# Kernel optimization log

Hardware: AMD Instinct MI355X
Metric: run time of the kernel (lower is better)

Reference implementation:

```python
import jax, jax.numpy as jnp
import numpy as np

HIDDEN = 2048
NUM_HEADS = 16
HEAD_DIM = HIDDEN // NUM_HEADS
ROPE_THETA = 10000.0


def _rope_cos_sin(n, dtype):
    # Llama-style: inv_freq over even indices, emb = concat([freqs, freqs])
    inv_freq = 1.0 / (ROPE_THETA ** (jnp.arange(0, HEAD_DIM, 2, dtype=jnp.float32) / HEAD_DIM))
    pos = jnp.arange(n, dtype=jnp.float32)
    freqs = pos[:, None] * inv_freq[None, :]          # [N, HEAD_DIM/2]
    emb = jnp.concatenate([freqs, freqs], axis=-1)    # [N, HEAD_DIM]
    return jnp.cos(emb).astype(dtype), jnp.sin(emb).astype(dtype)


def _rotate_half(x):
    x1, x2 = jnp.split(x, 2, axis=-1)
    return jnp.concatenate([-x2, x1], axis=-1)


def setup_inputs() -> dict:
    key = jax.random.key(0)
    ks = jax.random.split(key, 5)
    B, N, D = 2, 2048, HIDDEN
    s = 1.0 / np.sqrt(D)
    return {
        "x": jax.random.normal(ks[0], (B, N, D), jnp.float32),
        "Wq": jax.random.normal(ks[1], (D, D), jnp.float32) * s,
        "Wk": jax.random.normal(ks[2], (D, D), jnp.float32) * s,
        "Wv": jax.random.normal(ks[3], (D, D), jnp.float32) * s,
        "Wo": jax.random.normal(ks[4], (D, D), jnp.float32) * s,
    }


def reference(x, Wq, Wk, Wv, Wo):
    B, N, D = x.shape
    scale = HEAD_DIM ** -0.5

    def proj(W):  # nn.Linear(bias=False): x @ W.T, then split heads -> [B,H,N,hd]
        return (x @ W.T).reshape(B, N, NUM_HEADS, HEAD_DIM).transpose(0, 2, 1, 3)

    q, k, v = proj(Wq), proj(Wk), proj(Wv)

    cos, sin = _rope_cos_sin(N, x.dtype)  # [N, HEAD_DIM]
    cos = cos[None, None]                 # broadcast over B, H
    sin = sin[None, None]
    q = q * cos + _rotate_half(q) * sin
    k = k * cos + _rotate_half(k) * sin

    attn = jnp.einsum("bhqd,bhkd->bhqk", q, k) * scale  # full N x N scores
    attn = jax.nn.softmax(attn, axis=-1)                 # dropout p=0 -> identity
    out = jnp.einsum("bhqk,bhkd->bhqd", attn, v)
    out = out.transpose(0, 2, 1, 3).reshape(B, N, D)
    return out @ Wo.T
```

## Files before the change

kernel.cpp:

```cpp
#include <hip/hip_runtime.h>
#include <hip/hip_bf16.h>
#include <math.h>

typedef short bf16x8 __attribute__((ext_vector_type(8)));
typedef short bf16x4 __attribute__((ext_vector_type(4)));
typedef float f32x4 __attribute__((ext_vector_type(4)));

#define NSEQ 2048
#define DMODEL 2048
#define NH 16
#define HD 128
#define BATCH 2
#define MROWS 4096

__device__ __forceinline__ unsigned short f2b(float f) {
    __hip_bfloat16 h = __float2bfloat16(f);
    return *reinterpret_cast<unsigned short*>(&h);
}
__device__ __forceinline__ float b2f(unsigned short u) {
    __hip_bfloat16 h;
    *reinterpret_cast<unsigned short*>(&h) = u;
    return __bfloat162float(h);
}

__device__ __forceinline__ void gld_lds16(const unsigned short* g, unsigned short* l) {
    __builtin_amdgcn_global_load_lds(
        (const __attribute__((address_space(1))) unsigned int*)(const void*)g,
        (__attribute__((address_space(3))) unsigned int*)(void*)l,
        16, 0, 0);
}

__global__ __launch_bounds__(256) void cast_all_kernel(const float* __restrict__ x,
                                                       const float* __restrict__ wq,
                                                       const float* __restrict__ wk,
                                                       const float* __restrict__ wv,
                                                       const float* __restrict__ wo,
                                                       unsigned short* __restrict__ xb,
                                                       unsigned short* __restrict__ wqb) {
    int bid = blockIdx.x;
    const float* src;
    unsigned short* dst;
    int off;
    if (bid < 4096) {
        src = x; dst = xb; off = bid;
    } else {
        int w = (bid - 4096) >> 11;
        src = (w == 0) ? wq : (w == 1) ? wk : (w == 2) ? wv : wo;
        dst = wqb + (size_t)w * 4194304;
        off = (bid - 4096) & 2047;
    }
    int i = (off * 256 + threadIdx.x) * 8;
    float4 a = *(const float4*)(src + i);
    float4 b = *(const float4*)(src + i + 4);
    union { unsigned short u[8]; uint4 v; } tmp;
    tmp.u[0] = f2b(a.x); tmp.u[1] = f2b(a.y); tmp.u[2] = f2b(a.z); tmp.u[3] = f2b(a.w);
    tmp.u[4] = f2b(b.x); tmp.u[5] = f2b(b.y); tmp.u[6] = f2b(b.z); tmp.u[7] = f2b(b.w);
    *(uint4*)(dst + i) = tmp.v;
}

__global__ __launch_bounds__(256) void gemm_qkv(const unsigned short* __restrict__ A,
                                                const unsigned short* __restrict__ Bw,
                                                unsigned short* __restrict__ qk,
                                                unsigned short* __restrict__ vt) {
    __shared__ unsigned short sA[128 * 32];
    __shared__ unsigned short sB[128 * 32];
    const int K = DMODEL;
    const int tid = threadIdx.x;
    const int wave = tid >> 6, lane = tid & 63;
    const int m0 = blockIdx.y * 128, n0 = blockIdx.x * 128;
    const int wm = wave * 32;

    f32x4 acc[2][8] = {};

    const int srow = wave * 32 + (lane >> 2);
    const int scol = (lane & 3) * 8;
    const unsigned short* Ag = A + (size_t)(m0 + srow) * K + scol;
    const unsigned short* Bg = Bw + (size_t)(n0 + srow) * K + scol;
    unsigned short* sA0 = &sA[(wave * 32) * 32];
    unsigned short* sA1 = &sA[(wave * 32 + 16) * 32];
    unsigned short* sB0 = &sB[(wave * 32) * 32];
    unsigned short* sB1 = &sB[(wave * 32 + 16) * 32];
    const int fr = lane & 15, fo = (lane >> 4) * 8;

    for (int kb = 0; kb < K; kb += 32) {
        gld_lds16(Ag + kb, sA0);
        gld_lds16(Ag + (size_t)16 * K + kb, sA1);
        gld_lds16(Bg + kb, sB0);
        gld_lds16(Bg + (size_t)16 * K + kb, sB1);
        __syncthreads();
        bf16x8 af[2], bfr[8];
        #pragma unroll
        for (int mt = 0; mt < 2; mt++)
            af[mt] = *(const bf16x8*)&sA[(wm + mt * 16 + fr) * 32 + fo];
        #pragma unroll
        for (int nt = 0; nt < 8; nt++)
            bfr[nt] = *(const bf16x8*)&sB[(nt * 16 + fr) * 32 + fo];
        #pragma unroll
        for (int mt = 0; mt < 2; mt++)
            #pragma unroll
            for (int nt = 0; nt < 8; nt++)
                acc[mt][nt] = __builtin_amdgcn_mfma_f32_16x16x32_bf16(af[mt], bfr[nt], acc[mt][nt], 0, 0, 0);
        __syncthreads();
    }

    const int g4 = (lane >> 4) * 4, c0 = lane & 15;
    if (n0 < 4096) {
        const float scale = (n0 < 2048) ? 0.08838834764831845f : 1.0f;
        unsigned short* dst = qk + (size_t)(n0 >> 11) * 8388608;
        const int colbase = n0 & 2047;
        float invf[4];
        #pragma unroll
        for (int nt = 0; nt < 4; nt++)
            invf[nt] = exp2f((float)(nt * 16 + c0) * -0.2076205059304545f);
        #pragma unroll
        for (int mt = 0; mt < 2; mt++) {
            #pragma unroll
            for (int r = 0; r < 4; r++) {
                int row = m0 + wm + mt * 16 + g4 + r;
                float nf = (float)(row & (NSEQ - 1));
                size_t rbase = (size_t)row * 2048 + colbase + c0;
                #pragma unroll
                for (int nt = 0; nt < 4; nt++) {
                    float sv, cv;
                    __sincosf(nf * invf[nt], &sv, &cv);
                    float lo = acc[mt][nt][r], hi = acc[mt][nt + 4][r];
                    dst[rbase + nt * 16]      = f2b((lo * cv - hi * sv) * scale);
                    dst[rbase + nt * 16 + 64] = f2b((hi * cv + lo * sv) * scale);
                }
            }
        }
    } else {
        #pragma unroll
        for (int mt = 0; mt < 2; mt++) {
            int mbase = m0 + wm + mt * 16 + g4;
            int bb = mbase >> 11;
            int nn = mbase & 2047;
            #pragma unroll
            for (int nt = 0; nt < 8; nt++) {
                int d = n0 - 4096 + nt * 16 + c0;
                union { unsigned short u[4]; uint2 v; } o;
                #pragma unroll
                for (int r = 0; r < 4; r++) o.u[r] = f2b(acc[mt][nt][r]);
                *(uint2*)(vt + ((size_t)(bb * 2048 + d)) * 2048 + nn) = o.v;
            }
        }
    }
}

__global__ __launch_bounds__(256) void gemm_out(const unsigned short* __restrict__ A,
                                                const unsigned short* __restrict__ Bw,
                                                float* __restrict__ Cf) {
    __shared__ unsigned short sA[64 * 32];
    __shared__ unsigned short sB[128 * 32];
    const int K = DMODEL, Nn = DMODEL;
    const int tid = threadIdx.x;
    const int wave = tid >> 6, lane = tid & 63;
    const int m0 = blockIdx.y * 64, n0 = blockIdx.x * 128;
    const int wm = (wave >> 1) * 32, wn = (wave & 1) * 64;

    f32x4 acc[2][4] = {};

    const int srowA = wave * 16 + (lane >> 2);
    const int srowB = wave * 32 + (lane >> 2);
    const int scol = (lane & 3) * 8;
    const unsigned short* Ag = A + (size_t)(m0 + srowA) * K + scol;
    const unsigned short* Bg = Bw + (size_t)(n0 + srowB) * K + scol;
    unsigned short* sA0 = &sA[(wave * 16) * 32];
    unsigned short* sB0 = &sB[(wave * 32) * 32];
    unsigned short* sB1 = &sB[(wave * 32 + 16) * 32];
    const int fr = lane & 15, fo = (lane >> 4) * 8;

    for (int kb = 0; kb < K; kb += 32) {
        gld_lds16(Ag + kb, sA0);
        gld_lds16(Bg + kb, sB0);
        gld_lds16(Bg + (size_t)16 * K + kb, sB1);
        __syncthreads();
        bf16x8 af[2], bfr[4];
        #pragma unroll
        for (int mt = 0; mt < 2; mt++)
            af[mt] = *(const bf16x8*)&sA[(wm + mt * 16 + fr) * 32 + fo];
        #pragma unroll
        for (int nt = 0; nt < 4; nt++)
            bfr[nt] = *(const bf16x8*)&sB[(wn + nt * 16 + fr) * 32 + fo];
        #pragma unroll
        for (int mt = 0; mt < 2; mt++)
            #pragma unroll
            for (int nt = 0; nt < 4; nt++)
                acc[mt][nt] = __builtin_amdgcn_mfma_f32_16x16x32_bf16(af[mt], bfr[nt], acc[mt][nt], 0, 0, 0);
        __syncthreads();
    }

    const int g4 = (lane >> 4) * 4, c0 = lane & 15;
    #pragma unroll
    for (int mt = 0; mt < 2; mt++)
        #pragma unroll
        for (int nt = 0; nt < 4; nt++) {
            int col = n0 + wn + nt * 16 + c0;
            #pragma unroll
            for (int r = 0; r < 4; r++) {
                int row = m0 + wm + mt * 16 + g4 + r;
                Cf[(size_t)row * Nn + col] = acc[mt][nt][r];
            }
        }
}

__global__ __launch_bounds__(256) void attn_kernel(const unsigned short* __restrict__ Q,
                                                   const unsigned short* __restrict__ Kg,
                                                   const unsigned short* __restrict__ Vt,
                                                   unsigned short* __restrict__ O) {
    __shared__ unsigned short sK[64 * 136];
    __shared__ unsigned short sV[128 * 88];

    const int bh = blockIdx.x;
    const int b = bh >> 4, h = bh & 15;
    const int qt = blockIdx.y;
    const int tid = threadIdx.x, wave = tid >> 6, lane = tid & 63;
    const int c0 = lane & 15, grp = lane >> 4;

    bf16x8 qf[2][4];
    {
        const unsigned short* Qbase = Q + (size_t)(b * NSEQ + qt * 128 + wave * 32 + c0) * DMODEL + h * HD + grp * 8;
        #pragma unroll
        for (int nt = 0; nt < 2; nt++)
            #pragma unroll
            for (int ks = 0; ks < 4; ks++)
                qf[nt][ks] = *(const bf16x8*)(Qbase + (size_t)nt * 16 * DMODEL + ks * 32);
    }

    f32x4 oacc[8][2] = {};
    float lsum[2] = {0.f, 0.f};

    const unsigned short* Kbase = Kg + (size_t)(b * NSEQ) * DMODEL + h * HD;
    const unsigned short* Vbase = Vt + (size_t)(bh * HD) * NSEQ;

    for (int kv0 = 0; kv0 < NSEQ; kv0 += 64) {
        __syncthreads();
        #pragma unroll
        for (int i = 0; i < 4; i++) {
            int fl = i * 256 + tid;
            int rr = fl >> 4, cc = fl & 15;
            *(uint4*)&sK[rr * 136 + cc * 8] = *(const uint4*)(Kbase + (size_t)(kv0 + rr) * DMODEL + cc * 8);
        }
        #pragma unroll
        for (int i = 0; i < 4; i++) {
            int fl = i * 256 + tid;
            int rr = fl >> 3, cc = fl & 7;
            *(uint4*)&sV[rr * 88 + cc * 8] = *(const uint4*)(Vbase + (size_t)rr * NSEQ + kv0 + cc * 8);
        }
        __syncthreads();

        f32x4 s[4][2] = {};
        #pragma unroll
        for (int ks = 0; ks < 4; ks++) {
            bf16x8 kf[4];
            #pragma unroll
            for (int mt = 0; mt < 4; mt++)
                kf[mt] = *(const bf16x8*)&sK[(mt * 16 + c0) * 136 + ks * 32 + grp * 8];
            #pragma unroll
            for (int mt = 0; mt < 4; mt++)
                #pragma unroll
                for (int nt = 0; nt < 2; nt++)
                    s[mt][nt] = __builtin_amdgcn_mfma_f32_16x16x32_bf16(kf[mt], qf[nt][ks], s[mt][nt], 0, 0, 0);
        }

        bf16x4 pk[4][2];
        #pragma unroll
        for (int mt = 0; mt < 4; mt++)
            #pragma unroll
            for (int nt = 0; nt < 2; nt++) {
                float p0 = __expf(s[mt][nt][0]);
                float p1 = __expf(s[mt][nt][1]);
                float p2 = __expf(s[mt][nt][2]);
                float p3 = __expf(s[mt][nt][3]);
                lsum[nt] += (p0 + p1) + (p2 + p3);
                bf16x4 t;
                t[0] = (short)f2b(p0); t[1] = (short)f2b(p1);
                t[2] = (short)f2b(p2); t[3] = (short)f2b(p3);
                pk[mt][nt] = t;
            }

        #pragma unroll
        for (int mtK = 0; mtK < 4; mtK++) {
            bf16x4 va[8];
            #pragma unroll
            for (int mo = 0; mo < 8; mo++)
                va[mo] = *(const bf16x4*)&sV[(mo * 16 + c0) * 88 + mtK * 16 + grp * 4];
            #pragma unroll
            for (int mo = 0; mo < 8; mo++)
                #pragma unroll
                for (int nt = 0; nt < 2; nt++)
                    oacc[mo][nt] = __builtin_amdgcn_mfma_f32_16x16x16bf16_1k(va[mo], pk[mtK][nt], oacc[mo][nt], 0, 0, 0);
        }
    }

    float invl[2];
    #pragma unroll
    for (int nt = 0; nt < 2; nt++) {
        float li = lsum[nt];
        li += __shfl_xor(li, 16);
        li += __shfl_xor(li, 32);
        invl[nt] = 1.0f / li;
    }
    #pragma unroll
    for (int mo = 0; mo < 8; mo++)
        #pragma unroll
        for (int nt = 0; nt < 2; nt++) {
            union { unsigned short u[4]; uint2 v; } o;
            #pragma unroll
            for (int r = 0; r < 4; r++)
                o.u[r] = f2b(oacc[mo][nt][r] * invl[nt]);
            int row = b * NSEQ + qt * 128 + wave * 32 + nt * 16 + c0;
            int col = h * HD + mo * 16 + grp * 4;
            *(uint2*)(O + (size_t)row * DMODEL + col) = o.v;
        }
}

extern "C" void kernel_launch(void* const* d_in, const int* in_sizes, int n_in,
                              void* d_out, int out_size, void* d_ws, size_t ws_size,
                              hipStream_t stream) {
    const float* x  = (const float*)d_in[0];
    const float* Wq = (const float*)d_in[1];
    const float* Wk = (const float*)d_in[2];
    const float* Wv = (const float*)d_in[3];
    const float* Wo = (const float*)d_in[4];

    char* ws = (char*)d_ws;
    unsigned short* xb  = (unsigned short*)(ws);
    unsigned short* wqb = (unsigned short*)(ws + 16777216);
    unsigned short* wob = (unsigned short*)(ws + 16777216 + 3 * 8388608);
    unsigned short* qb  = (unsigned short*)(ws + 50331648);
    unsigned short* kb  = (unsigned short*)(ws + 67108864);
    unsigned short* vt  = (unsigned short*)(ws + 83886080);

    cast_all_kernel<<<12288, 256, 0, stream>>>(x, Wq, Wk, Wv, Wo, xb, wqb);

    gemm_qkv<<<dim3(48, 32), 256, 0, stream>>>(xb, wqb, qb, vt);

    attn_kernel<<<dim3(32, 16), 256, 0, stream>>>(qb, kb, vt, xb);

    gemm_out<<<dim3(16, 64), 256, 0, stream>>>(xb, wob, (float*)d_out);
}
```

Measured before the change: 414.8 us.

## Enlarge output GEMM tile to 128x128 with K=64 steps and XOR-swizzled LDS

Makes the output projection GEMM compute 128x128 tiles per block instead of 64x128, with each wave holding a 4x4 set of MFMA accumulators. It also processes 64 elements of K per iteration instead of 32. An XOR swizzle on the LDS chunk index is intended to avoid bank conflicts on the fragment reads. The aim is more reuse per loaded byte and fewer barriers per FLOP, at the cost of more registers and LDS per block and half as many blocks (512).

After: 388.8 us. 6.3% less time.

```diff
diff --git a/kernel.cpp b/kernel.cpp
--- a/kernel.cpp
+++ b/kernel.cpp
@@ -150,49 +150,55 @@
 __global__ __launch_bounds__(256) void gemm_out(const unsigned short* __restrict__ A,
                                                 const unsigned short* __restrict__ Bw,
                                                 float* __restrict__ Cf) {
-    __shared__ unsigned short sA[64 * 32];
-    __shared__ unsigned short sB[128 * 32];
+    __shared__ unsigned short sA[128 * 64];
+    __shared__ unsigned short sB[128 * 64];
     const int K = DMODEL, Nn = DMODEL;
     const int tid = threadIdx.x;
     const int wave = tid >> 6, lane = tid & 63;
-    const int m0 = blockIdx.y * 64, n0 = blockIdx.x * 128;
-    const int wm = (wave >> 1) * 32, wn = (wave & 1) * 64;
-
-    f32x4 acc[2][4] = {};
-
-    const int srowA = wave * 16 + (lane >> 2);
-    const int srowB = wave * 32 + (lane >> 2);
-    const int scol = (lane & 3) * 8;
-    const unsigned short* Ag = A + (size_t)(m0 + srowA) * K + scol;
-    const unsigned short* Bg = Bw + (size_t)(n0 + srowB) * K + scol;
-    unsigned short* sA0 = &sA[(wave * 16) * 32];
-    unsigned short* sB0 = &sB[(wave * 32) * 32];
-    unsigned short* sB1 = &sB[(wave * 32 + 16) * 32];
-    const int fr = lane & 15, fo = (lane >> 4) * 8;
-
-    for (int kb = 0; kb < K; kb += 32) {
-        gld_lds16(Ag + kb, sA0);
-        gld_lds16(Bg + kb, sB0);
-        gld_lds16(Bg + (size_t)16 * K + kb, sB1);
-        __syncthreads();
-        bf16x8 af[2], bfr[4];
-        #pragma unroll
-        for (int mt = 0; mt < 2; mt++)
-            af[mt] = *(const bf16x8*)&sA[(wm + mt * 16 + fr) * 32 + fo];
-        #pragma unroll
-        for (int nt = 0; nt < 4; nt++)
-            bfr[nt] = *(const bf16x8*)&sB[(wn + nt * 16 + fr) * 32 + fo];
-        #pragma unroll
-        for (int mt = 0; mt < 2; mt++)
+    const int m0 = blockIdx.y * 128, n0 = blockIdx.x * 128;
+    const int wm = (wave >> 1) * 64, wn = (wave & 1) * 64;
+
+    f32x4 acc[4][4] = {};
+
+    const int srowoff = wave * 8 + (lane >> 3);
+    const int gchunk = ((lane & 7) ^ ((lane >> 3) & 7)) * 8;
+    const unsigned short* Ag = A + (size_t)(m0 + srowoff) * K + gchunk;
+    const unsigned short* Bg = Bw + (size_t)(n0 + srowoff) * K + gchunk;
+    unsigned short* sAw = &sA[(wave * 8) * 64];
+    unsigned short* sBw = &sB[(wave * 8) * 64];
+
+    const int fr = lane & 15, grp = lane >> 4;
+    const int swz = fr & 7;
+
+    for (int kb = 0; kb < K; kb += 64) {
+        #pragma unroll
+        for (int i = 0; i < 4; i++)
+            gld_lds16(Ag + (size_t)(i * 32) * K + kb, sAw + i * 32 * 64);
+        #pragma unroll
+        for (int i = 0; i < 4; i++)
+            gld_lds16(Bg + (size_t)(i * 32) * K + kb, sBw + i * 32 * 64);
+        __syncthreads();
+        #pragma unroll
+        for (int ks = 0; ks < 2; ks++) {
+            bf16x8 af[4], bfr[4];
+            #pragma unroll
+            for (int mt = 0; mt < 4; mt++)
+                af[mt] = *(const bf16x8*)&sA[(wm + mt * 16 + fr) * 64 + (((ks * 4 + grp) ^ swz) << 3)];
             #pragma unroll
             for (int nt = 0; nt < 4; nt++)
-                acc[mt][nt] = __builtin_amdgcn_mfma_f32_16x16x32_bf16(af[mt], bfr[nt], acc[mt][nt], 0, 0, 0);
+                bfr[nt] = *(const bf16x8*)&sB[(wn + nt * 16 + fr) * 64 + (((ks * 4 + grp) ^ swz) << 3)];
+            #pragma unroll
+            for (int mt = 0; mt < 4; mt++)
+                #pragma unroll
+                for (int nt = 0; nt < 4; nt++)
+                    acc[mt][nt] = __builtin_amdgcn_mfma_f32_16x16x32_bf16(af[mt], bfr[nt], acc[mt][nt], 0, 0, 0);
+        }
         __syncthreads();
     }
 
     const int g4 = (lane >> 4) * 4, c0 = lane & 15;
     #pragma unroll
-    for (int mt = 0; mt < 2; mt++)
+    for (int mt = 0; mt < 4; mt++)
         #pragma unroll
         for (int nt = 0; nt < 4; nt++) {
             int col = n0 + wn + nt * 16 + c0;
@@ -338,5 +344,5 @@
 
     attn_kernel<<<dim3(32, 16), 256, 0, stream>>>(qb, kb, vt, xb);
 
-    gemm_out<<<dim3(16, 64), 256, 0, stream>>>(xb, wob, (float*)d_out);
-}
+    gemm_out<<<dim3(16, 32), 256, 0, stream>>>(xb, wob, (float*)d_out);
+}
```
